# Kernel optimization log

Hardware: AMD Instinct MI355X
Metric: run time of the kernel (lower is better)

Reference implementation:

```python
import jax, jax.numpy as jnp
import numpy as np
import math

N_EMBD = 768
N_HEAD = 12
B, T = 4, 2048
HEAD_DIM = N_EMBD // N_HEAD


def new_gelu(x):
    # GPT-2 tanh approximation of GELU (NewGELUActivation)
    c = math.sqrt(2.0 / math.pi)
    return 0.5 * x * (1.0 + jnp.tanh(c * (x + 0.044715 * jnp.power(x, 3.0))))


def layer_norm(x, g, b, eps=1e-5):
    mu = jnp.mean(x, axis=-1, keepdims=True)
    var = jnp.mean(jnp.square(x - mu), axis=-1, keepdims=True)
    return (x - mu) * jax.lax.rsqrt(var + eps) * g + b


def setup_inputs() -> dict:
    key = jax.random.key(0)
    ks = jax.random.split(key, 12)
    s = 0.02
    return {
        "x": jax.random.normal(ks[0], (B, T, N_EMBD), dtype=jnp.float32),
        "ln1_g": jnp.ones((N_EMBD,), jnp.float32),
        "ln1_b": jnp.zeros((N_EMBD,), jnp.float32),
        "W_attn": jax.random.normal(ks[1], (N_EMBD, 3 * N_EMBD), jnp.float32) * s,
        "b_attn": jnp.zeros((3 * N_EMBD,), jnp.float32),
        "W_proj": jax.random.normal(ks[2], (N_EMBD, N_EMBD), jnp.float32) * s,
        "b_proj": jnp.zeros((N_EMBD,), jnp.float32),
        "ln2_g": jnp.ones((N_EMBD,), jnp.float32),
        "ln2_b": jnp.zeros((N_EMBD,), jnp.float32),
        "W_fc": jax.random.normal(ks[3], (N_EMBD, 4 * N_EMBD), jnp.float32) * s,
        "b_fc": jnp.zeros((4 * N_EMBD,), jnp.float32),
        "W_fc2": jax.random.normal(ks[4], (4 * N_EMBD, N_EMBD), jnp.float32) * s,
        "b_fc2": jnp.zeros((N_EMBD,), jnp.float32),
    }


def block_forward(x, ln1_g, ln1_b, W_attn, b_attn, W_proj, b_proj,
                  ln2_g, ln2_b, W_fc, b_fc, W_fc2, b_fc2):
    # ---- attention sublayer (pre-LN) ----
    h = layer_norm(x, ln1_g, ln1_b)
    qkv = h @ W_attn + b_attn                      # [B,T,3C]
    q, k, v = jnp.split(qkv, 3, axis=-1)
    q = q.reshape(B, T, N_HEAD, HEAD_DIM).transpose(0, 2, 1, 3)  # [B,H,T,D]
    k = k.reshape(B, T, N_HEAD, HEAD_DIM).transpose(0, 2, 1, 3)
    v = v.reshape(B, T, N_HEAD, HEAD_DIM).transpose(0, 2, 1, 3)
    scores = jnp.einsum('bhqd,bhkd->bhqk', q, k) / math.sqrt(HEAD_DIM)
    causal = jnp.tril(jnp.ones((T, T), dtype=bool))
    scores = jnp.where(causal[None, None, :, :], scores, -jnp.inf)
    attn = jax.nn.softmax(scores, axis=-1)
    y = jnp.einsum('bhqk,bhkd->bhqd', attn, v)      # [B,H,T,D]
    y = y.transpose(0, 2, 1, 3).reshape(B, T, N_EMBD)
    y = y @ W_proj + b_proj
    x = x + y
    # ---- MLP sublayer ----
    h = layer_norm(x, ln2_g, ln2_b)
    h = new_gelu(h @ W_fc + b_fc)
    h = h @ W_fc2 + b_fc2
    return x + h


def reference(x, ln1_g, ln1_b, W_attn, b_attn, W_proj, b_proj,
              ln2_g, ln2_b, W_fc, b_fc, W_fc2, b_fc2):
    return block_forward(x, ln1_g, ln1_b, W_attn, b_attn, W_proj, b_proj,
                         ln2_g, ln2_b, W_fc, b_fc, W_fc2, b_fc2)
```

## Files before the change

kernel.cpp:

```cpp
#include <hip/hip_runtime.h>
#include <hip/hip_bf16.h>

typedef __attribute__((ext_vector_type(8))) short short8;
typedef __attribute__((ext_vector_type(4))) float f32x4;
typedef __attribute__((ext_vector_type(8))) unsigned short u16x8;
typedef __attribute__((ext_vector_type(4))) unsigned short u16x4;

#define MFMA16(A, B, C) __builtin_amdgcn_mfma_f32_16x16x32_bf16(A, B, C, 0, 0, 0)

static __device__ __forceinline__ unsigned short f2bf(float f) {
    unsigned int u = __builtin_bit_cast(unsigned int, f);
    u += 0x7FFF + ((u >> 16) & 1);
    return (unsigned short)(u >> 16);
}

static __device__ __forceinline__ unsigned int cvt_pk_bf16(float a, float b) {
    unsigned int r;
    asm("v_cvt_pk_bf16_f32 %0, %1, %2" : "=v"(r) : "v"(a), "v"(b));
    return r;
}

static __device__ __forceinline__ float gelu_f(float v) {
    const float k1 = 2.3022077646f;
    const float k2 = 0.1029432207f;
    float t = __builtin_amdgcn_exp2f(-(k1 * v + k2 * v * v * v));
    return v * __builtin_amdgcn_rcpf(1.0f + t);
}

typedef const __attribute__((address_space(1))) unsigned int* gas_t;
typedef __attribute__((address_space(3))) unsigned int* las_t;
static __device__ __forceinline__ void gl_lds16(const void* g, void* l) {
    __builtin_amdgcn_global_load_lds((gas_t)g, (las_t)l, 16, 0, 0);
}

__global__ void wtrans(const float* __restrict__ W, unsigned short* __restrict__ Wt,
                       int K, int N) {
    __shared__ float tl[32][33];
    const int n0 = blockIdx.x * 32, k0 = blockIdx.y * 32;
    const int tx = threadIdx.x, ty = threadIdx.y;
#pragma unroll
    for (int i = 0; i < 4; i++)
        tl[ty + 8 * i][tx] = W[(long)(k0 + ty + 8 * i) * N + n0 + tx];
    __syncthreads();
#pragma unroll
    for (int i = 0; i < 4; i++)
        Wt[(long)(n0 + ty + 8 * i) * K + k0 + tx] = f2bf(tl[tx][ty + 8 * i]);
}

__global__ __launch_bounds__(256)
void ln_fwd(const float* __restrict__ x, const float* __restrict__ gw,
            const float* __restrict__ bw, unsigned short* __restrict__ out) {
    const int row = blockIdx.x * 4 + (threadIdx.x >> 6);
    const int ln = threadIdx.x & 63;
    const float4* xr = (const float4*)(x + (long)row * 768);
    float4 v[3];
    float s = 0.f;
#pragma unroll
    for (int j = 0; j < 3; j++) {
        v[j] = xr[ln + 64 * j];
        s += v[j].x + v[j].y + v[j].z + v[j].w;
    }
#pragma unroll
    for (int off = 32; off >= 1; off >>= 1) s += __shfl_xor(s, off);
    const float mean = s * (1.0f / 768.0f);
    float sq = 0.f;
#pragma unroll
    for (int j = 0; j < 3; j++) {
        float a = v[j].x - mean, b = v[j].y - mean, c = v[j].z - mean, d = v[j].w - mean;
        sq += a * a + b * b + c * c + d * d;
    }
#pragma unroll
    for (int off = 32; off >= 1; off >>= 1) sq += __shfl_xor(sq, off);
    const float rstd = rsqrtf(sq * (1.0f / 768.0f) + 1e-5f);
#pragma unroll
    for (int j = 0; j < 3; j++) {
        const int c = ln + 64 * j;
        float4 gg = ((const float4*)gw)[c];
        float4 bb = ((const float4*)bw)[c];
        u16x4 o;
        o[0] = f2bf((v[j].x - mean) * rstd * gg.x + bb.x);
        o[1] = f2bf((v[j].y - mean) * rstd * gg.y + bb.y);
        o[2] = f2bf((v[j].z - mean) * rstd * gg.z + bb.z);
        o[3] = f2bf((v[j].w - mean) * rstd * gg.w + bb.w);
        *(u16x4*)(out + (long)row * 768 + c * 4) = o;
    }
}

template <int MODE, int BN>
__global__ __launch_bounds__(256)
void gemm_bt(const unsigned short* __restrict__ A, const unsigned short* __restrict__ Bt,
             const float* __restrict__ bias, const float* __restrict__ resid,
             void* __restrict__ Out, int M, int N, int K) {
    constexpr int NW = BN / 32;
    constexpr int BUF = (128 + BN) * 32;
    constexpr int STN = (BN == 128) ? 132 : 68;
    constexpr int BYTES_MAIN = 2 * BUF * 2;
    constexpr int BYTES_ST = 64 * STN * 4;
    constexpr int BYTES = BYTES_MAIN > BYTES_ST ? BYTES_MAIN : BYTES_ST;
    __shared__ char smem[BYTES];
    unsigned short* ubase = (unsigned short*)smem;
    float* st = (float*)smem;

    const int tid = threadIdx.x;
    const int wv = tid >> 6, ln = tid & 63;
    const int wr = wv >> 1, wc = wv & 1;
    const int g = ln >> 4, r = ln & 15;
    const int sr = ln >> 2, sc = ln & 3;
    const int ssw = sc ^ (sr & 3);
    const long mbase = (long)blockIdx.x * 128;
    const long nbase = (long)blockIdx.y * BN;

    f32x4 acc[4][NW];
    const f32x4 zero = {0.f, 0.f, 0.f, 0.f};
#pragma unroll
    for (int m = 0; m < 4; m++)
#pragma unroll
        for (int n = 0; n < NW; n++) acc[m][n] = zero;

    const int nt = K >> 5;
#pragma unroll
    for (int p = 0; p < 2; p++)
        gl_lds16(A + (mbase + p * 64 + wv * 16 + sr) * (long)K + ssw * 8,
                 ubase + (p * 64 + wv * 16) * 32);
#pragma unroll
    for (int p = 0; p < BN / 64; p++)
        gl_lds16(Bt + (nbase + p * 64 + wv * 16 + sr) * (long)K + ssw * 8,
                 ubase + 128 * 32 + (p * 64 + wv * 16) * 32);
    __syncthreads();

    const int cxr = r & 3;
    for (int t = 0; t < nt; t++) {
        const unsigned short* cbuf = ubase + (t & 1) * BUF;
        if (t + 1 < nt) {
            unsigned short* nbuf = ubase + ((t + 1) & 1) * BUF;
            const long k0 = (long)(t + 1) << 5;
#pragma unroll
            for (int p = 0; p < 2; p++)
                gl_lds16(A + (mbase + p * 64 + wv * 16 + sr) * (long)K + k0 + ssw * 8,
                         nbuf + (p * 64 + wv * 16) * 32);
#pragma unroll
            for (int p = 0; p < BN / 64; p++)
                gl_lds16(Bt + (nbase + p * 64 + wv * 16 + sr) * (long)K + k0 + ssw * 8,
                         nbuf + 128 * 32 + (p * 64 + wv * 16) * 32);
        }
        short8 af[4], bfr[NW];
#pragma unroll
        for (int m = 0; m < 4; m++)
            af[m] = *(const short8*)(cbuf + (wr * 64 + m * 16 + r) * 32 + ((g ^ cxr) * 8));
#pragma unroll
        for (int n = 0; n < NW; n++)
            bfr[n] = *(const short8*)(cbuf + 128 * 32 + (wc * (BN / 2) + n * 16 + r) * 32 + ((g ^ cxr) * 8));
#pragma unroll
        for (int m = 0; m < 4; m++)
#pragma unroll
            for (int n = 0; n < NW; n++) acc[m][n] = MFMA16(af[m], bfr[n], acc[m][n]);
        __syncthreads();
    }

    const int tr = tid >> 2, seg = tid & 3;
#pragma unroll 1
    for (int half = 0; half < 2; half++) {
        __syncthreads();
        if (wr == half) {
#pragma unroll
            for (int m = 0; m < 4; m++)
#pragma unroll
                for (int n = 0; n < NW; n++)
#pragma unroll
                    for (int i = 0; i < 4; i++)
                        st[(m * 16 + g * 4 + i) * STN + wc * (BN / 2) + n * 16 + r] = acc[m][n][i];
        }
        __syncthreads();
        const long row = mbase + half * 64 + tr;
        if constexpr (BN == 128) {
            const long cb = nbase + seg * 32;
            if constexpr (MODE == 1 || MODE == 3) {
                const float qs = (MODE == 1 && nbase < 768) ? 0.18033688011112042f : 1.0f;
                unsigned short* op = (unsigned short*)Out + row * N + cb;
#pragma unroll
                for (int u2 = 0; u2 < 4; u2++) {
                    float4 a = *(const float4*)(st + tr * STN + seg * 32 + u2 * 8);
                    float4 b = *(const float4*)(st + tr * STN + seg * 32 + u2 * 8 + 4);
                    float4 ba = ((const float4*)bias)[(cb >> 2) + u2 * 2];
                    float4 bb = ((const float4*)bias)[(cb >> 2) + u2 * 2 + 1];
                    a.x += ba.x; a.y += ba.y; a.z += ba.z; a.w += ba.w;
                    b.x += bb.x; b.y += bb.y; b.z += bb.z; b.w += bb.w;
                    if constexpr (MODE == 1) {
                        a.x *= qs; a.y *= qs; a.z *= qs; a.w *= qs;
                        b.x *= qs; b.y *= qs; b.z *= qs; b.w *= qs;
                    } else {
                        a.x = gelu_f(a.x); a.y = gelu_f(a.y); a.z = gelu_f(a.z); a.w = gelu_f(a.w);
                        b.x = gelu_f(b.x); b.y = gelu_f(b.y); b.z = gelu_f(b.z); b.w = gelu_f(b.w);
                    }
                    uint4 w;
                    w.x = cvt_pk_bf16(a.x, a.y);
                    w.y = cvt_pk_bf16(a.z, a.w);
                    w.z = cvt_pk_bf16(b.x, b.y);
                    w.w = cvt_pk_bf16(b.z, b.w);
                    *(uint4*)(op + u2 * 8) = w;
                }
            } else {
                float* op = (float*)Out + row * N + cb;
                const float* rp = resid + row * N + cb;
#pragma unroll
                for (int u = 0; u < 8; u++) {
                    float4 a = *(const float4*)(st + tr * STN + seg * 32 + u * 4);
                    float4 ba = ((const float4*)bias)[(cb >> 2) + u];
                    float4 rr = ((const float4*)rp)[u];
                    a.x += ba.x + rr.x; a.y += ba.y + rr.y;
                    a.z += ba.z + rr.z; a.w += ba.w + rr.w;
                    ((float4*)op)[u] = a;
                }
            }
        } else {
            const long cb = nbase + seg * 16;
            float* op = (float*)Out + row * N + cb;
            const float* rp = resid + row * N + cb;
#pragma unroll
            for (int u = 0; u < 4; u++) {
                float4 a = *(const float4*)(st + tr * STN + seg * 16 + u * 4);
                float4 ba = ((const float4*)bias)[(cb >> 2) + u];
                float4 rr = ((const float4*)rp)[u];
                a.x += ba.x + rr.x; a.y += ba.y + rr.y;
                a.z += ba.z + rr.z; a.w += ba.w + rr.w;
                ((float4*)op)[u] = a;
            }
        }
    }
}

__global__ __launch_bounds__(256)
void vtrans(const unsigned short* __restrict__ qkv, unsigned short* __restrict__ vT) {
    const int t0 = blockIdx.x * 64;
    const int bh = blockIdx.y;
    const int b = bh / 12, h = bh % 12;
    __shared__ unsigned short tl[64 * 72];
    const int tid = threadIdx.x;
#pragma unroll
    for (int p = 0; p < 2; p++) {
        int idx = p * 256 + tid;
        int row = idx >> 3, blk = idx & 7;
        int sb = (blk + row) % 9;
        *(u16x8*)(tl + row * 72 + sb * 8) =
            *(const u16x8*)(qkv + ((long)(b * 2048 + t0 + row)) * 2304 + 1536 + h * 64 + blk * 8);
    }
    __syncthreads();
#pragma unroll
    for (int p = 0; p < 2; p++) {
        int idx = p * 256 + tid;
        int d = idx >> 3, tc = (idx & 7) * 8;
        u16x8 v;
#pragma unroll
        for (int j = 0; j < 8; j++) {
            int t = tc + j;
            int sb = ((d >> 3) + t) % 9;
            v[j] = tl[t * 72 + sb * 8 + (d & 7)];
        }
        *(u16x8*)(vT + ((long)(bh * 64 + d)) * 2048 + t0 + tc) = v;
    }
}

__global__ __launch_bounds__(256)
void attn_fwd(const unsigned short* __restrict__ qkv, const unsigned short* __restrict__ vT,
              unsigned short* __restrict__ y) {
    const int pair = blockIdx.x;
    const int bh = blockIdx.y;
    const int b = bh / 12, h = bh % 12;
    __shared__ unsigned short Kl[2 * 64 * 64], Vl[2 * 64 * 64], Pl[64 * 72];
    const int tid = threadIdx.x;
    const int wv = tid >> 6, ln = tid & 63;
    const int g = ln >> 4, r = ln & 15;
    const int lr = ln >> 3, l8 = ln & 7;
    const int sw = l8 ^ lr;
    const int rx = r & 7;
    const f32x4 zero = {0.f, 0.f, 0.f, 0.f};

#pragma unroll 1
    for (int qi = 0; qi < 2; qi++) {
        const int qt = qi ? (31 - pair) : pair;
        const int q0 = qt * 64;
        const int q = wv * 16 + r;
        const long qoff = ((long)(b * 2048 + q0 + q)) * 2304 + h * 64;
        short8 bq0 = *(const short8*)(qkv + qoff + g * 8);
        short8 bq1 = *(const short8*)(qkv + qoff + 32 + g * 8);

        float mrow = -1e30f, lrow = 0.0f;
        f32x4 oacc[4];
#pragma unroll
        for (int f = 0; f < 4; f++) oacc[f] = zero;

#pragma unroll
        for (int p = 0; p < 2; p++) {
            const int row = wv * 8 + p * 32 + lr;
            gl_lds16(qkv + ((long)(b * 2048 + row)) * 2304 + 768 + h * 64 + sw * 8,
                     (char*)Kl + (wv * 8 + p * 32) * 128);
            gl_lds16(vT + ((long)(bh * 64 + row)) * 2048 + sw * 8,
                     (char*)Vl + (wv * 8 + p * 32) * 128);
        }
        __syncthreads();

        for (int kt = 0; kt <= qt; ++kt) {
            const unsigned short* Kb = Kl + (kt & 1) * 4096;
            const unsigned short* Vb = Vl + (kt & 1) * 4096;
            if (kt < qt) {
                char* Kn = (char*)Kl + ((kt + 1) & 1) * 8192;
                char* Vn = (char*)Vl + ((kt + 1) & 1) * 8192;
#pragma unroll
                for (int p = 0; p < 2; p++) {
                    const int row = wv * 8 + p * 32 + lr;
                    gl_lds16(qkv + ((long)(b * 2048 + (kt + 1) * 64 + row)) * 2304 + 768 + h * 64 + sw * 8,
                             Kn + (wv * 8 + p * 32) * 128);
                    gl_lds16(vT + ((long)(bh * 64 + row)) * 2048 + (kt + 1) * 64 + sw * 8,
                             Vn + (wv * 8 + p * 32) * 128);
                }
            }

            f32x4 s[4];
#pragma unroll
            for (int kf = 0; kf < 4; kf++) {
                short8 a0 = *(const short8*)(Kb + (kf * 16 + r) * 64 + (g ^ rx) * 8);
                short8 a1 = *(const short8*)(Kb + (kf * 16 + r) * 64 + ((g + 4) ^ rx) * 8);
                s[kf] = MFMA16(a0, bq0, zero);
                s[kf] = MFMA16(a1, bq1, s[kf]);
            }
            if (kt == qt) {
#pragma unroll
                for (int kf = 0; kf < 4; kf++)
#pragma unroll
                    for (int i = 0; i < 4; i++)
                        if (kf * 16 + g * 4 + i > q) s[kf][i] = -1e30f;
            }
            float tmax = -1e30f;
#pragma unroll
            for (int kf = 0; kf < 4; kf++)
#pragma unroll
                for (int i = 0; i < 4; i++) tmax = fmaxf(tmax, s[kf][i]);
            tmax = fmaxf(tmax, __shfl_xor(tmax, 16));
            tmax = fmaxf(tmax, __shfl_xor(tmax, 32));
            if (__any(tmax > mrow + 6.0f)) {
                const float mnew = fmaxf(mrow, tmax);
                const float rs = __builtin_amdgcn_exp2f(mrow - mnew);
                lrow *= rs;
#pragma unroll
                for (int f = 0; f < 4; f++) oacc[f] *= rs;
                mrow = mnew;
            }
            float pv[4][4];
            float psum = 0.f;
#pragma unroll
            for (int kf = 0; kf < 4; kf++)
#pragma unroll
                for (int i = 0; i < 4; i++) {
                    pv[kf][i] = __builtin_amdgcn_exp2f(s[kf][i] - mrow);
                    psum += pv[kf][i];
                }
            psum += __shfl_xor(psum, 16);
            psum += __shfl_xor(psum, 32);
            lrow += psum;

#pragma unroll
            for (int kf = 0; kf < 4; kf++) {
                uint2 w;
                w.x = cvt_pk_bf16(pv[kf][0], pv[kf][1]);
                w.y = cvt_pk_bf16(pv[kf][2], pv[kf][3]);
                *(uint2*)(Pl + q * 72 + kf * 16 + g * 4) = w;
            }
            short8 pb0 = *(const short8*)(Pl + q * 72 + g * 8);
            short8 pb1 = *(const short8*)(Pl + q * 72 + 32 + g * 8);
#pragma unroll
            for (int f = 0; f < 4; f++) {
                short8 va0 = *(const short8*)(Vb + (f * 16 + r) * 64 + (g ^ rx) * 8);
                short8 va1 = *(const short8*)(Vb + (f * 16 + r) * 64 + ((g + 4) ^ rx) * 8);
                oacc[f] = MFMA16(va0, pb0, oacc[f]);
                oacc[f] = MFMA16(va1, pb1, oacc[f]);
            }
            __syncthreads();
        }

        const float inv = 1.0f / lrow;
#pragma unroll
        for (int f = 0; f < 4; f++) {
            uint2 w;
            w.x = cvt_pk_bf16(oacc[f][0] * inv, oacc[f][1] * inv);
            w.y = cvt_pk_bf16(oacc[f][2] * inv, oacc[f][3] * inv);
            *(uint2*)(Pl + q * 72 + f * 16 + g * 4) = w;
        }
        __syncthreads();
#pragma unroll
        for (int p = 0; p < 2; p++) {
            int idx = p * 256 + tid;
            int row = idx >> 3, cc = (idx & 7) * 8;
            *(u16x8*)(y + ((long)(b * 2048 + q0 + row)) * 768 + h * 64 + cc) =
                *(const u16x8*)(Pl + row * 72 + cc);
        }
        __syncthreads();
    }
}

extern "C" void kernel_launch(void* const* d_in, const int* in_sizes, int n_in,
                              void* d_out, int out_size, void* d_ws, size_t ws_size,
                              hipStream_t stream) {
    const float* x      = (const float*)d_in[0];
    const float* ln1_g  = (const float*)d_in[1];
    const float* ln1_b  = (const float*)d_in[2];
    const float* W_attn = (const float*)d_in[3];
    const float* b_attn = (const float*)d_in[4];
    const float* W_proj = (const float*)d_in[5];
    const float* b_proj = (const float*)d_in[6];
    const float* ln2_g  = (const float*)d_in[7];
    const float* ln2_b  = (const float*)d_in[8];
    const float* W_fc   = (const float*)d_in[9];
    const float* b_fc   = (const float*)d_in[10];
    const float* W_fc2  = (const float*)d_in[11];
    const float* b_fc2  = (const float*)d_in[12];

    char* ws = (char*)d_ws;
    size_t off = 0;
    auto alloc = [&](size_t bytes) -> char* {
        char* p = ws + off;
        off += (bytes + 255) & ~(size_t)255;
        return p;
    };
    unsigned short* WtA  = (unsigned short*)alloc((size_t)2304 * 768 * 2);
    unsigned short* WtP  = (unsigned short*)alloc((size_t)768 * 768 * 2);
    unsigned short* WtF  = (unsigned short*)alloc((size_t)3072 * 768 * 2);
    unsigned short* WtF2 = (unsigned short*)alloc((size_t)768 * 3072 * 2);
    unsigned short* bigA = (unsigned short*)alloc((size_t)8192 * 3072 * 2);
    float*          x1   = (float*)alloc((size_t)8192 * 768 * 4);
    unsigned short* bufD = (unsigned short*)alloc((size_t)8192 * 768 * 2);
    unsigned short* vT   = (unsigned short*)alloc((size_t)48 * 64 * 2048 * 2);

    wtrans<<<dim3(72, 24), dim3(32, 8), 0, stream>>>(W_attn, WtA, 768, 2304);
    wtrans<<<dim3(24, 24), dim3(32, 8), 0, stream>>>(W_proj, WtP, 768, 768);
    wtrans<<<dim3(96, 24), dim3(32, 8), 0, stream>>>(W_fc, WtF, 768, 3072);
    wtrans<<<dim3(24, 96), dim3(32, 8), 0, stream>>>(W_fc2, WtF2, 3072, 768);
    ln_fwd<<<2048, 256, 0, stream>>>(x, ln1_g, ln1_b, bufD);
    gemm_bt<1, 128><<<dim3(64, 18), 256, 0, stream>>>(bufD, WtA, b_attn, nullptr, bigA, 8192, 2304, 768);
    vtrans<<<dim3(32, 48), 256, 0, stream>>>(bigA, vT);
    attn_fwd<<<dim3(16, 48), 256, 0, stream>>>(bigA, vT, bufD);
    gemm_bt<2, 64><<<dim3(64, 12), 256, 0, stream>>>(bufD, WtP, b_proj, x, x1, 8192, 768, 768);
    ln_fwd<<<2048, 256, 0, stream>>>(x1, ln2_g, ln2_b, bufD);
    gemm_bt<3, 128><<<dim3(64, 24), 256, 0, stream>>>(bufD, WtF, b_fc, nullptr, bigA, 8192, 3072, 768);
    gemm_bt<4, 64><<<dim3(64, 12), 256, 0, stream>>>(bigA, WtF2, b_fc2, x1, (float*)d_out, 8192, 768, 3072);
}
```

Baseline: 292.3 us.

## Fuse V transpose into QKV GEMM epilogue and change LDS swizzle

```diff
diff --git a/kernel.cpp b/kernel.cpp
--- a/kernel.cpp
+++ b/kernel.cpp
@@ -90,7 +90,8 @@
 __global__ __launch_bounds__(256)
 void gemm_bt(const unsigned short* __restrict__ A, const unsigned short* __restrict__ Bt,
              const float* __restrict__ bias, const float* __restrict__ resid,
-             void* __restrict__ Out, int M, int N, int K) {
+             void* __restrict__ Out, unsigned short* __restrict__ vT,
+             int M, int N, int K) {
     constexpr int NW = BN / 32;
     constexpr int BUF = (128 + BN) * 32;
     constexpr int STN = (BN == 128) ? 132 : 68;
@@ -106,7 +107,7 @@
     const int wr = wv >> 1, wc = wv & 1;
     const int g = ln >> 4, r = ln & 15;
     const int sr = ln >> 2, sc = ln & 3;
-    const int ssw = sc ^ (sr & 3);
+    const int ssw = sc ^ ((sr >> 1) & 3);
     const long mbase = (long)blockIdx.x * 128;
     const long nbase = (long)blockIdx.y * BN;
 
@@ -128,7 +129,7 @@
                  ubase + 128 * 32 + (p * 64 + wv * 16) * 32);
     __syncthreads();
 
-    const int cxr = r & 3;
+    const int cx = (r >> 1) & 3;
     for (int t = 0; t < nt; t++) {
         const unsigned short* cbuf = ubase + (t & 1) * BUF;
         if (t + 1 < nt) {
@@ -146,10 +147,10 @@
         short8 af[4], bfr[NW];
 #pragma unroll
         for (int m = 0; m < 4; m++)
-            af[m] = *(const short8*)(cbuf + (wr * 64 + m * 16 + r) * 32 + ((g ^ cxr) * 8));
+            af[m] = *(const short8*)(cbuf + (wr * 64 + m * 16 + r) * 32 + ((g ^ cx) * 8));
 #pragma unroll
         for (int n = 0; n < NW; n++)
-            bfr[n] = *(const short8*)(cbuf + 128 * 32 + (wc * (BN / 2) + n * 16 + r) * 32 + ((g ^ cxr) * 8));
+            bfr[n] = *(const short8*)(cbuf + 128 * 32 + (wc * (BN / 2) + n * 16 + r) * 32 + ((g ^ cx) * 8));
 #pragma unroll
         for (int m = 0; m < 4; m++)
 #pragma unroll
@@ -172,26 +173,38 @@
         }
         __syncthreads();
         const long row = mbase + half * 64 + tr;
-        if constexpr (BN == 128) {
-            const long cb = nbase + seg * 32;
-            if constexpr (MODE == 1 || MODE == 3) {
-                const float qs = (MODE == 1 && nbase < 768) ? 0.18033688011112042f : 1.0f;
+        if constexpr (MODE == 1) {
+            if (nbase >= 1536) {
+                const int tc = tid & 7;
+                const int d0 = tid >> 3;
+                const long bb = mbase >> 11;
+                const int tg0 = (int)(mbase & 2047) + half * 64 + tc * 8;
+#pragma unroll
+                for (int it = 0; it < 4; it++) {
+                    const int dl = it * 32 + d0;
+                    const int h = (int)((nbase - 1536) >> 6) + (dl >> 6);
+                    const int dd = dl & 63;
+                    const float bc = bias[nbase + dl];
+                    u16x8 o;
+#pragma unroll
+                    for (int j = 0; j < 8; j++)
+                        o[j] = f2bf(st[(tc * 8 + j) * STN + dl] + bc);
+                    *(u16x8*)(vT + ((bb * 12 + h) * 64 + dd) * 2048 + tg0) = o;
+                }
+            } else {
+                const float qs = (nbase < 768) ? 0.18033688011112042f : 1.0f;
+                const long cb = nbase + seg * 32;
                 unsigned short* op = (unsigned short*)Out + row * N + cb;
 #pragma unroll
                 for (int u2 = 0; u2 < 4; u2++) {
                     float4 a = *(const float4*)(st + tr * STN + seg * 32 + u2 * 8);
                     float4 b = *(const float4*)(st + tr * STN + seg * 32 + u2 * 8 + 4);
                     float4 ba = ((const float4*)bias)[(cb >> 2) + u2 * 2];
-                    float4 bb = ((const float4*)bias)[(cb >> 2) + u2 * 2 + 1];
-                    a.x += ba.x; a.y += ba.y; a.z += ba.z; a.w += ba.w;
-                    b.x += bb.x; b.y += bb.y; b.z += bb.z; b.w += bb.w;
-                    if constexpr (MODE == 1) {
-                        a.x *= qs; a.y *= qs; a.z *= qs; a.w *= qs;
-                        b.x *= qs; b.y *= qs; b.z *= qs; b.w *= qs;
-                    } else {
-                        a.x = gelu_f(a.x); a.y = gelu_f(a.y); a.z = gelu_f(a.z); a.w = gelu_f(a.w);
-                        b.x = gelu_f(b.x); b.y = gelu_f(b.y); b.z = gelu_f(b.z); b.w = gelu_f(b.w);
-                    }
+                    float4 bb2 = ((const float4*)bias)[(cb >> 2) + u2 * 2 + 1];
+                    a.x = (a.x + ba.x) * qs; a.y = (a.y + ba.y) * qs;
+                    a.z = (a.z + ba.z) * qs; a.w = (a.w + ba.w) * qs;
+                    b.x = (b.x + bb2.x) * qs; b.y = (b.y + bb2.y) * qs;
+                    b.z = (b.z + bb2.z) * qs; b.w = (b.w + bb2.w) * qs;
                     uint4 w;
                     w.x = cvt_pk_bf16(a.x, a.y);
                     w.y = cvt_pk_bf16(a.z, a.w);
@@ -199,18 +212,26 @@
                     w.w = cvt_pk_bf16(b.z, b.w);
                     *(uint4*)(op + u2 * 8) = w;
                 }
-            } else {
-                float* op = (float*)Out + row * N + cb;
-                const float* rp = resid + row * N + cb;
-#pragma unroll
-                for (int u = 0; u < 8; u++) {
-                    float4 a = *(const float4*)(st + tr * STN + seg * 32 + u * 4);
-                    float4 ba = ((const float4*)bias)[(cb >> 2) + u];
-                    float4 rr = ((const float4*)rp)[u];
-                    a.x += ba.x + rr.x; a.y += ba.y + rr.y;
-                    a.z += ba.z + rr.z; a.w += ba.w + rr.w;
-                    ((float4*)op)[u] = a;
-                }
+            }
+        } else if constexpr (MODE == 3) {
+            const long cb = nbase + seg * 32;
+            unsigned short* op = (unsigned short*)Out + row * N + cb;
+#pragma unroll
+            for (int u2 = 0; u2 < 4; u2++) {
+                float4 a = *(const float4*)(st + tr * STN + seg * 32 + u2 * 8);
+                float4 b = *(const float4*)(st + tr * STN + seg * 32 + u2 * 8 + 4);
+                float4 ba = ((const float4*)bias)[(cb >> 2) + u2 * 2];
+                float4 bb2 = ((const float4*)bias)[(cb >> 2) + u2 * 2 + 1];
+                a.x = gelu_f(a.x + ba.x); a.y = gelu_f(a.y + ba.y);
+                a.z = gelu_f(a.z + ba.z); a.w = gelu_f(a.w + ba.w);
+                b.x = gelu_f(b.x + bb2.x); b.y = gelu_f(b.y + bb2.y);
+                b.z = gelu_f(b.z + bb2.z); b.w = gelu_f(b.w + bb2.w);
+                uint4 w;
+                w.x = cvt_pk_bf16(a.x, a.y);
+                w.y = cvt_pk_bf16(a.z, a.w);
+                w.z = cvt_pk_bf16(b.x, b.y);
+                w.w = cvt_pk_bf16(b.z, b.w);
+                *(uint4*)(op + u2 * 8) = w;
             }
         } else {
             const long cb = nbase + seg * 16;
@@ -226,37 +247,6 @@
                 ((float4*)op)[u] = a;
             }
         }
-    }
-}
-
-__global__ __launch_bounds__(256)
-void vtrans(const unsigned short* __restrict__ qkv, unsigned short* __restrict__ vT) {
-    const int t0 = blockIdx.x * 64;
-    const int bh = blockIdx.y;
-    const int b = bh / 12, h = bh % 12;
-    __shared__ unsigned short tl[64 * 72];
-    const int tid = threadIdx.x;
-#pragma unroll
-    for (int p = 0; p < 2; p++) {
-        int idx = p * 256 + tid;
-        int row = idx >> 3, blk = idx & 7;
-        int sb = (blk + row) % 9;
-        *(u16x8*)(tl + row * 72 + sb * 8) =
-            *(const u16x8*)(qkv + ((long)(b * 2048 + t0 + row)) * 2304 + 1536 + h * 64 + blk * 8);
-    }
-    __syncthreads();
-#pragma unroll
-    for (int p = 0; p < 2; p++) {
-        int idx = p * 256 + tid;
-        int d = idx >> 3, tc = (idx & 7) * 8;
-        u16x8 v;
-#pragma unroll
-        for (int j = 0; j < 8; j++) {
-            int t = tc + j;
-            int sb = ((d >> 3) + t) % 9;
-            v[j] = tl[t * 72 + sb * 8 + (d & 7)];
-        }
-        *(u16x8*)(vT + ((long)(bh * 64 + d)) * 2048 + t0 + tc) = v;
     }
 }
 
@@ -435,11 +425,10 @@
     wtrans<<<dim3(96, 24), dim3(32, 8), 0, stream>>>(W_fc, WtF, 768, 3072);
     wtrans<<<dim3(24, 96), dim3(32, 8), 0, stream>>>(W_fc2, WtF2, 3072, 768);
     ln_fwd<<<2048, 256, 0, stream>>>(x, ln1_g, ln1_b, bufD);
-    gemm_bt<1, 128><<<dim3(64, 18), 256, 0, stream>>>(bufD, WtA, b_attn, nullptr, bigA, 8192, 2304, 768);
-    vtrans<<<dim3(32, 48), 256, 0, stream>>>(bigA, vT);
+    gemm_bt<1, 128><<<dim3(64, 18), 256, 0, stream>>>(bufD, WtA, b_attn, nullptr, bigA, vT, 8192, 2304, 768);
     attn_fwd<<<dim3(16, 48), 256, 0, stream>>>(bigA, vT, bufD);
-    gemm_bt<2, 64><<<dim3(64, 12), 256, 0, stream>>>(bufD, WtP, b_proj, x, x1, 8192, 768, 768);
+    gemm_bt<2, 64><<<dim3(64, 12), 256, 0, stream>>>(bufD, WtP, b_proj, x, x1, nullptr, 8192, 768, 768);
     ln_fwd<<<2048, 256, 0, stream>>>(x1, ln2_g, ln2_b, bufD);
-    gemm_bt<3, 128><<<dim3(64, 24), 256, 0, stream>>>(bufD, WtF, b_fc, nullptr, bigA, 8192, 3072, 768);
-    gemm_bt<4, 64><<<dim3(64, 12), 256, 0, stream>>>(bigA, WtF2, b_fc2, x1, (float*)d_out, 8192, 768, 3072);
-}
+    gemm_bt<3, 128><<<dim3(64, 24), 256, 0, stream>>>(bufD, WtF, b_fc, nullptr, bigA, nullptr, 8192, 3072, 768);
+    gemm_bt<4, 64><<<dim3(64, 12), 256, 0, stream>>>(bigA, WtF2, b_fc2, x1, (float*)d_out, nullptr, 8192, 768, 3072);
+}
```

Result: faster. 286.3 us (-2.0%).
